# Optimization experiments

Hardware: AMD Instinct MI355X
Metric: run time of the kernel (lower is better)

## Reference

```python
import jax, jax.numpy as jnp
import numpy as np

B, N, D = 8, 2048, 256
K = 8
NP = 1024  # num_pooled = ceil(N * 0.5)
EPS = 1e-8
TEMP = 1.0


def setup_inputs() -> dict:
    key = jax.random.key(0)
    k1, k2, k3, k4 = jax.random.split(key, 4)
    tokens = jax.random.normal(k1, (B, N, D), dtype=jnp.float32)
    timestamps = jax.random.uniform(k2, (B, N), dtype=jnp.float32)
    W1 = jax.random.normal(k3, (2 * D, 128), dtype=jnp.float32) * 0.02
    b1 = jnp.zeros((128,), dtype=jnp.float32)
    W2 = jax.random.normal(k4, (128, NP), dtype=jnp.float32) * 0.02
    b2 = jnp.zeros((NP,), dtype=jnp.float32)
    return {"tokens": tokens, "timestamps": timestamps, "W1": W1, "b1": b1, "W2": W2, "b2": b2}


def _build_adjacency(tokens):
    # mutual-kNN graph on cosine similarity -> [B, N, N] float 0/1
    tn = tokens / (jnp.linalg.norm(tokens, axis=-1, keepdims=True) + EPS)
    sim = jnp.einsum("bnd,bmd->bnm", tn, tn)
    sim = jnp.where(jnp.eye(N, dtype=bool)[None], -jnp.inf, sim)  # no self (add_self=False)
    _, idx = jax.lax.top_k(sim, K)  # [B, N, K]
    bi = jnp.arange(B)[:, None, None]
    ri = jnp.arange(N)[None, :, None]
    adj = jnp.zeros((B, N, N), dtype=bool).at[bi, ri, idx].set(True)
    adj = adj & jnp.swapaxes(adj, 1, 2)  # mutual
    return adj.astype(jnp.float32)


def reference(tokens, timestamps, W1, b1, W2, b2):
    adjacency = _build_adjacency(tokens)

    # degree-normalized aggregation (use_gnn=True)
    degree = jnp.clip(adjacency.sum(axis=-1, keepdims=True), 1.0, None)
    agg = jnp.matmul(adjacency / degree, tokens)  # [B, N, D]
    features = jnp.concatenate([tokens, agg], axis=-1)  # [B, N, 2D]

    # assignment MLP (Linear -> exact GELU -> Linear), softmax over clusters
    h = jax.nn.gelu(features @ W1 + b1, approximate=False)
    logits = h @ W2 + b2  # [B, N, NP]
    assign = jax.nn.softmax(logits / TEMP, axis=-1)

    # soft-assignment pooling
    pooled_tokens = jnp.einsum("bnp,bnd->bpd", assign, tokens)  # [B, NP, D]
    pooled_t = jnp.einsum("bnp,bn->bp", assign, timestamps)  # [B, NP]

    # reorder pooled tokens by pooled timestamp
    sort_idx = jnp.argsort(pooled_t, axis=-1)
    pooled_tokens = jnp.take_along_axis(pooled_tokens, sort_idx[..., None], axis=1)
    pooled_t = jnp.take_along_axis(pooled_t, sort_idx, axis=1)

    # auxiliary losses
    assign_st = jnp.einsum("bnp,bmp->bnm", assign, assign)
    link_loss = jnp.mean((assign_st - adjacency) ** 2)
    entropy = jnp.mean(-jnp.sum(assign * jnp.log(assign + EPS), axis=-1))

    return pooled_tokens, pooled_t, link_loss, entropy
```

## Files before the change

### kernel.cpp

```cpp
#include <hip/hip_runtime.h>
#include <math.h>

#define B_ 8
#define N_ 2048
#define D_ 256
#define K_ 8
#define NP_ 1024
#define H_ 128
#define EPS_ 1e-8f
#define NEG_INF_ (-1e30f)

typedef unsigned int uint;
typedef unsigned short ushort;
typedef __attribute__((ext_vector_type(4))) float f32x4;
typedef __attribute__((ext_vector_type(8))) short short8;

__device__ __forceinline__ float gelu_exact(float x) {
    return 0.5f * x * (1.0f + erff(x * 0.70710678118654752440f));
}

__device__ __forceinline__ float dot4(float4 a, float4 b) {
    return a.x * b.x + a.y * b.y + a.z * b.z + a.w * b.w;
}

__device__ __forceinline__ ushort f2bf(float f) {
    uint u = __float_as_uint(f);
    u = (u + 0x7FFFu + ((u >> 16) & 1u)) >> 16;
    return (ushort)u;
}

__device__ __forceinline__ void gll16(const void* g, void* l) {
    __builtin_amdgcn_global_load_lds(
        (const __attribute__((address_space(1))) unsigned int*)g,
        (__attribute__((address_space(3))) unsigned int*)l, 16, 0, 0);
}

__device__ __forceinline__ float bsum256(float* red, int t, float v) {
    red[t] = v;
    __syncthreads();
#pragma unroll
    for (int s = 128; s > 0; s >>= 1) {
        if (t < s) red[t] += red[t + s];
        __syncthreads();
    }
    float r = red[0];
    __syncthreads();
    return r;
}

__device__ __forceinline__ float bmax256(float* red, int t, float v) {
    red[t] = v;
    __syncthreads();
#pragma unroll
    for (int s = 128; s > 0; s >>= 1) {
        if (t < s) red[t] = fmaxf(red[t], red[t + s]);
        __syncthreads();
    }
    float r = red[0];
    __syncthreads();
    return r;
}

__device__ __forceinline__ uint mono16(uint v) {
    return (v & 0x8000u) ? ((~v) & 0xFFFFu) : (v | 0x8000u);
}

__global__ __launch_bounds__(256) void k_norm(const float* __restrict__ tokens,
                                              float* __restrict__ tn,
                                              ushort* __restrict__ tnbf) {
    int row = blockIdx.x;
    int t = threadIdx.x;
    __shared__ float red[256];
    float x = tokens[(size_t)row * D_ + t];
    float ss = bsum256(red, t, x * x);
    float nrm = sqrtf(ss) + EPS_;
    float y = x / nrm;
    tn[(size_t)row * D_ + t] = y;
    tnbf[(size_t)row * D_ + t] = f2bf(y);
}

#define SCW_ 72
#define INSK_(L) { bool in_ = key > L; uint tm_ = L; L = in_ ? key : L; key = in_ ? tm_ : key; }
#define INS16_ INSK_(l0) INSK_(l1) INSK_(l2) INSK_(l3) INSK_(l4) INSK_(l5) INSK_(l6) INSK_(l7) \
               INSK_(l8) INSK_(l9) INSK_(l10) INSK_(l11) INSK_(l12) INSK_(l13) INSK_(l14) INSK_(l15)
#define INSM_ INSK_(m0) INSK_(m1) INSK_(m2) INSK_(m3) INSK_(m4) INSK_(m5) INSK_(m6) INSK_(m7) \
              INSK_(m8) INSK_(m9) INSK_(m10) INSK_(m11) INSK_(m12) INSK_(m13) INSK_(m14) INSK_(m15)

__global__ __launch_bounds__(256) void k_simtop(const ushort* __restrict__ tnbf,
                                                int* __restrict__ cands) {
    __shared__ __align__(16) char lds[43264];
    char* Bs = lds + 8192;
    ushort* sc = (ushort*)(lds + 40960);
    uint* mg = (uint*)(lds + 8192);

    int bid = blockIdx.x;
    int b = bid & 7;
    int panel = bid >> 3;
    int i0 = panel * 16;
    int t = threadIdx.x;
    int lane = t & 63;
    int wv = t >> 6;
    const char* tbb = (const char*)(tnbf + (size_t)b * N_ * D_);

#pragma unroll
    for (int c = 0; c < 2; ++c) {
        int e = (wv * 2 + c) * 64 + lane;
        int row = e >> 5, g = e & 31;
        gll16(tbb + (size_t)(i0 + row) * 512 + ((g ^ (row & 15)) << 4),
              lds + (wv * 2 + c) * 1024);
    }
#pragma unroll
    for (int c = 0; c < 8; ++c) {
        int e = (wv * 8 + c) * 64 + lane;
        int row = e >> 5, g = e & 31;
        gll16(tbb + (size_t)row * 512 + ((g ^ (row & 15)) << 4),
              Bs + (wv * 8 + c) * 1024);
    }
    asm volatile("s_waitcnt vmcnt(0)" ::: "memory");
    __syncthreads();

    int selrow = t >> 4;
    int selcs = t & 15;
    int gi = i0 + selrow;
    uint l0=0,l1=0,l2=0,l3=0,l4=0,l5=0,l6=0,l7=0,l8=0,l9=0,l10=0,l11=0,l12=0,l13=0,l14=0,l15=0;

    int arow = lane & 15;
    int brow = wv * 16 + (lane & 15);
    int scw = ((lane >> 4) * 4) * SCW_ + wv * 16 + (lane & 15);

    for (int jt = 0; jt < 32; ++jt) {
        f32x4 acc = (f32x4){0.f, 0.f, 0.f, 0.f};
#pragma unroll
        for (int ks = 0; ks < 8; ++ks) {
            int u = ks * 4 + (lane >> 4);
            short8 af = *(const short8*)(lds + arow * 512 + ((u ^ arow) << 4));
            short8 bf = *(const short8*)(Bs + brow * 512 + ((u ^ (lane & 15)) << 4));
            acc = __builtin_amdgcn_mfma_f32_16x16x32_bf16(af, bf, acc, 0, 0, 0);
        }
#pragma unroll
        for (int v = 0; v < 4; ++v) sc[scw + v * SCW_] = f2bf(acc[v]);
        __syncthreads();

        if (jt < 31) {
#pragma unroll
            for (int c = 0; c < 8; ++c) {
                int e = (wv * 8 + c) * 64 + lane;
                int row = e >> 5, g = e & 31;
                gll16(tbb + (size_t)((jt + 1) * 64 + row) * 512 + ((g ^ (row & 15)) << 4),
                      Bs + (wv * 8 + c) * 1024);
            }
        }
        int j0 = jt * 64;
        int sbase = selrow * SCW_;
#pragma unroll
        for (int jj = 0; jj < 4; ++jj) {
            int col = selcs + jj * 16;
            int j = j0 + col;
            uint sv = sc[sbase + col];
            if (j != gi) {
                uint key = (mono16(sv) << 16) | (65535u - (uint)j);
                if (key > l15) { INS16_ }
            }
        }
        asm volatile("s_waitcnt vmcnt(0)" ::: "memory");
        __syncthreads();
    }

    uint* ml = mg + (size_t)t * 17;
    ml[0]=l0; ml[1]=l1; ml[2]=l2; ml[3]=l3; ml[4]=l4; ml[5]=l5; ml[6]=l6; ml[7]=l7;
    ml[8]=l8; ml[9]=l9; ml[10]=l10; ml[11]=l11; ml[12]=l12; ml[13]=l13; ml[14]=l14; ml[15]=l15;
    __syncthreads();
    if (selcs == 0) {
        uint m0=0,m1=0,m2=0,m3=0,m4=0,m5=0,m6=0,m7=0,m8=0,m9=0,m10=0,m11=0,m12=0,m13=0,m14=0,m15=0;
        const uint* base = mg + (size_t)(selrow * 16) * 17;
#pragma unroll
        for (int s2 = 0; s2 < 16; ++s2) {
            const uint* lp = base + s2 * 17;
            for (int q = 0; q < 16; ++q) {
                uint key = lp[q];
                if (key <= m15) break;
                INSM_
            }
        }
        int* crow = cands + ((size_t)b * N_ + gi) * 16;
        crow[0]=(int)(65535u-(m0&0xFFFFu));   crow[1]=(int)(65535u-(m1&0xFFFFu));
        crow[2]=(int)(65535u-(m2&0xFFFFu));   crow[3]=(int)(65535u-(m3&0xFFFFu));
        crow[4]=(int)(65535u-(m4&0xFFFFu));   crow[5]=(int)(65535u-(m5&0xFFFFu));
        crow[6]=(int)(65535u-(m6&0xFFFFu));   crow[7]=(int)(65535u-(m7&0xFFFFu));
        crow[8]=(int)(65535u-(m8&0xFFFFu));   crow[9]=(int)(65535u-(m9&0xFFFFu));
        crow[10]=(int)(65535u-(m10&0xFFFFu)); crow[11]=(int)(65535u-(m11&0xFFFFu));
        crow[12]=(int)(65535u-(m12&0xFFFFu)); crow[13]=(int)(65535u-(m13&0xFFFFu));
        crow[14]=(int)(65535u-(m14&0xFFFFu)); crow[15]=(int)(65535u-(m15&0xFFFFu));
    }
}

__global__ __launch_bounds__(64) void k_rescore(const float* __restrict__ tn,
                                                const int* __restrict__ cands,
                                                int* __restrict__ topk) {
    int row = blockIdx.x;
    int b = row >> 11;
    int lane = threadIdx.x;
    int j = cands[(size_t)row * 16 + (lane & 15)];
    float s = 0.f;
    if (lane < 16) {
        const float* ti = tn + (size_t)row * D_;
        const float* tj = tn + ((size_t)(b << 11) + j) * D_;
        for (int d = 0; d < D_; d += 4) {
            float4 u = *(const float4*)(tj + d);
            float4 w = *(const float4*)(ti + d);
            s += dot4(u, w);
        }
    }
    float dv[16];
    int jv[16];
#pragma unroll
    for (int c = 0; c < 16; ++c) {
        dv[c] = __shfl(s, c);
        jv[c] = __shfl(j, c);
    }
    uint used = 0;
    for (int r = 0; r < 8; ++r) {
        float bv = -1e38f;
        int bj = 1 << 30, bc = -1;
#pragma unroll
        for (int c = 0; c < 16; ++c) {
            bool av = !(used & (1u << c));
            bool better = av && (dv[c] > bv || (dv[c] == bv && jv[c] < bj));
            bv = better ? dv[c] : bv;
            bj = better ? jv[c] : bj;
            bc = better ? c : bc;
        }
        used |= 1u << bc;
        if (lane == 0) topk[(size_t)row * K_ + r] = bj;
    }
}

__global__ __launch_bounds__(64) void k_adj_agg(const float* __restrict__ tokens,
                                                const int* __restrict__ topk,
                                                int* __restrict__ nbr,
                                                int* __restrict__ deg,
                                                float* __restrict__ agg) {
    int row = blockIdx.x;
    int b = row >> 11;
    int i = row & (N_ - 1);
    int t = threadIdx.x;
    __shared__ int s_cand[K_];
    __shared__ int s_nbr[K_];
    __shared__ int s_deg;
    if (t < K_) {
        int j = topk[(size_t)row * K_ + t];
        const int* tj = topk + ((size_t)(b * N_ + j)) * K_;
        bool mut = false;
#pragma unroll
        for (int k = 0; k < K_; ++k) mut = mut || (tj[k] == i);
        s_cand[t] = mut ? j : -1;
    }
    __syncthreads();
    if (t == 0) {
        int d = 0;
#pragma unroll
        for (int k = 0; k < K_; ++k)
            if (s_cand[k] >= 0) s_nbr[d++] = s_cand[k];
        s_deg = d;
    }
    __syncthreads();
    int dgi = s_deg;
    const float* tb = tokens + (size_t)b * N_ * D_;
    float a0 = 0, a1 = 0, a2 = 0, a3 = 0;
    for (int k = 0; k < dgi; ++k) {
        float4 v = *(const float4*)(tb + (size_t)s_nbr[k] * D_ + t * 4);
        a0 += v.x; a1 += v.y; a2 += v.z; a3 += v.w;
    }
    float inv = 1.0f / (float)(dgi > 0 ? dgi : 1);
    *(float4*)(agg + (size_t)row * D_ + t * 4) = make_float4(a0 * inv, a1 * inv, a2 * inv, a3 * inv);
    if (t < K_) nbr[(size_t)row * K_ + t] = (t < dgi) ? s_nbr[t] : -1;
    if (t == 0) deg[row] = dgi;
}

__global__ __launch_bounds__(256) void k_tokT(const float* __restrict__ tokens,
                                              ushort* __restrict__ tokT) {
    int b = blockIdx.z;
    int n0 = blockIdx.x * 32, d0 = blockIdx.y * 32;
    __shared__ float tile[32][33];
    int t = threadIdx.x;
#pragma unroll
    for (int q = 0; q < 4; ++q) {
        int e = q * 256 + t;
        int r = e >> 5, c = e & 31;
        tile[r][c] = tokens[((size_t)b * N_ + n0 + r) * D_ + d0 + c];
    }
    __syncthreads();
#pragma unroll
    for (int q = 0; q < 4; ++q) {
        int e = q * 256 + t;
        int r = e >> 5, c = e & 31;
        tokT[((size_t)b * D_ + d0 + r) * N_ + n0 + c] = f2bf(tile[c][r]);
    }
}

__global__ __launch_bounds__(256) void k_asT(const float* __restrict__ assign,
                                             ushort* __restrict__ assignT) {
    int b = blockIdx.z;
    int n0 = blockIdx.x * 32, p0 = blockIdx.y * 32;
    __shared__ float tile[32][33];
    int t = threadIdx.x;
#pragma unroll
    for (int q = 0; q < 4; ++q) {
        int e = q * 256 + t;
        int r = e >> 5, c = e & 31;
        tile[r][c] = assign[((size_t)b * N_ + n0 + r) * NP_ + p0 + c];
    }
    __syncthreads();
#pragma unroll
    for (int q = 0; q < 4; ++q) {
        int e = q * 256 + t;
        int r = e >> 5, c = e & 31;
        assignT[((size_t)b * NP_ + p0 + r) * N_ + n0 + c] = f2bf(tile[c][r]);
    }
}

__global__ __launch_bounds__(256) void k_mlp1(const float* __restrict__ tokens,
                                              const float* __restrict__ agg,
                                              const float* __restrict__ W1,
                                              const float* __restrict__ b1,
                                              float* __restrict__ h) {
    int row0 = blockIdx.x * 16;
    int t = threadIdx.x;
    int col = t & 127;
    int half = t >> 7;
    __shared__ float feat[16][2 * D_];
    for (int e = t; e < 16 * 2 * D_; e += 256) {
        int r = e >> 9, c = e & 511;
        feat[r][c] = (c < D_) ? tokens[(size_t)(row0 + r) * D_ + c]
                              : agg[(size_t)(row0 + r) * D_ + (c - D_)];
    }
    __syncthreads();
    const float* fr = &feat[half * 8][0];
    float bias = b1[col];
    float a0 = bias, a1 = bias, a2 = bias, a3 = bias, a4 = bias, a5 = bias, a6 = bias, a7 = bias;
    for (int i = 0; i < 2 * D_; i += 4) {
        float w0 = W1[(size_t)(i + 0) * H_ + col];
        float w1 = W1[(size_t)(i + 1) * H_ + col];
        float w2 = W1[(size_t)(i + 2) * H_ + col];
        float w3 = W1[(size_t)(i + 3) * H_ + col];
        float4 f0 = *(const float4*)(fr + 0 * 512 + i);
        float4 f1 = *(const float4*)(fr + 1 * 512 + i);
        float4 f2 = *(const float4*)(fr + 2 * 512 + i);
        float4 f3 = *(const float4*)(fr + 3 * 512 + i);
        float4 f4 = *(const float4*)(fr + 4 * 512 + i);
        float4 f5 = *(const float4*)(fr + 5 * 512 + i);
        float4 f6 = *(const float4*)(fr + 6 * 512 + i);
        float4 f7 = *(const float4*)(fr + 7 * 512 + i);
        a0 += f0.x * w0; a0 += f0.y * w1; a0 += f0.z * w2; a0 += f0.w * w3;
        a1 += f1.x * w0; a1 += f1.y * w1; a1 += f1.z * w2; a1 += f1.w * w3;
        a2 += f2.x * w0; a2 += f2.y * w1; a2 += f2.z * w2; a2 += f2.w * w3;
        a3 += f3.x * w0; a3 += f3.y * w1; a3 += f3.z * w2; a3 += f3.w * w3;
        a4 += f4.x * w0; a4 += f4.y * w1; a4 += f4.z * w2; a4 += f4.w * w3;
        a5 += f5.x * w0; a5 += f5.y * w1; a5 += f5.z * w2; a5 += f5.w * w3;
        a6 += f6.x * w0; a6 += f6.y * w1; a6 += f6.z * w2; a6 += f6.w * w3;
        a7 += f7.x * w0; a7 += f7.y * w1; a7 += f7.z * w2; a7 += f7.w * w3;
    }
    int rb = row0 + half * 8;
    h[(size_t)(rb + 0) * H_ + col] = gelu_exact(a0);
    h[(size_t)(rb + 1) * H_ + col] = gelu_exact(a1);
    h[(size_t)(rb + 2) * H_ + col] = gelu_exact(a2);
    h[(size_t)(rb + 3) * H_ + col] = gelu_exact(a3);
    h[(size_t)(rb + 4) * H_ + col] = gelu_exact(a4);
    h[(size_t)(rb + 5) * H_ + col] = gelu_exact(a5);
    h[(size_t)(rb + 6) * H_ + col] = gelu_exact(a6);
    h[(size_t)(rb + 7) * H_ + col] = gelu_exact(a7);
}

__global__ __launch_bounds__(256) void k_mlp2f(const float* __restrict__ hmat,
                                               const float* __restrict__ W2,
                                               const float* __restrict__ b2,
                                               float* __restrict__ assign,
                                               float* __restrict__ ent_partial) {
    int row0 = blockIdx.x * 16;
    int t = threadIdx.x;
    __shared__ float hsT[128 * 17];
    __shared__ float red2[16][256];
    __shared__ float red[256];
    for (int e = t; e < 16 * H_; e += 256) {
        int r = e >> 7, i = e & 127;
        hsT[i * 17 + r] = hmat[(size_t)row0 * H_ + e];
    }
    __syncthreads();
    float acc[16][4];
#pragma unroll
    for (int s = 0; s < 4; ++s) {
        float bb = b2[s * 256 + t];
#pragma unroll
        for (int r = 0; r < 16; ++r) acc[r][s] = bb;
    }
#pragma unroll 2
    for (int i = 0; i < H_; ++i) {
        float w0 = W2[(size_t)i * NP_ + t];
        float w1 = W2[(size_t)i * NP_ + 256 + t];
        float w2 = W2[(size_t)i * NP_ + 512 + t];
        float w3 = W2[(size_t)i * NP_ + 768 + t];
        float hv[16];
        *(float4*)&hv[0] = *(const float4*)&hsT[i * 17 + 0];
        *(float4*)&hv[4] = *(const float4*)&hsT[i * 17 + 4];
        *(float4*)&hv[8] = *(const float4*)&hsT[i * 17 + 8];
        *(float4*)&hv[12] = *(const float4*)&hsT[i * 17 + 12];
#pragma unroll
        for (int r = 0; r < 16; ++r) {
            acc[r][0] += hv[r] * w0; acc[r][1] += hv[r] * w1;
            acc[r][2] += hv[r] * w2; acc[r][3] += hv[r] * w3;
        }
    }
#pragma unroll
    for (int r = 0; r < 16; ++r)
        red2[r][t] = fmaxf(fmaxf(acc[r][0], acc[r][1]), fmaxf(acc[r][2], acc[r][3]));
    __syncthreads();
#pragma unroll
    for (int s = 128; s > 0; s >>= 1) {
        if (t < s) {
#pragma unroll
            for (int r = 0; r < 16; ++r) red2[r][t] = fmaxf(red2[r][t], red2[r][t + s]);
        }
        __syncthreads();
    }
#pragma unroll
    for (int r = 0; r < 16; ++r) {
        float m = red2[r][0];
        acc[r][0] -= m; acc[r][1] -= m; acc[r][2] -= m; acc[r][3] -= m;
    }
    __syncthreads();
#pragma unroll
    for (int r = 0; r < 16; ++r)
        red2[r][t] = expf(acc[r][0]) + expf(acc[r][1]) + expf(acc[r][2]) + expf(acc[r][3]);
    __syncthreads();
#pragma unroll
    for (int s = 128; s > 0; s >>= 1) {
        if (t < s) {
#pragma unroll
            for (int r = 0; r < 16; ++r) red2[r][t] += red2[r][t + s];
        }
        __syncthreads();
    }
    float entv = 0.f;
#pragma unroll
    for (int r = 0; r < 16; ++r) {
        float tot = red2[r][0];
        float inv = 1.0f / tot;
        float p0 = expf(acc[r][0]) * inv, p1 = expf(acc[r][1]) * inv;
        float p2 = expf(acc[r][2]) * inv, p3 = expf(acc[r][3]) * inv;
        float* arow = assign + (size_t)(row0 + r) * NP_;
        arow[t] = p0; arow[256 + t] = p1; arow[512 + t] = p2; arow[768 + t] = p3;
        entv -= p0 * logf(p0 + EPS_) + p1 * logf(p1 + EPS_) + p2 * logf(p2 + EPS_) + p3 * logf(p3 + EPS_);
    }
    float bs = bsum256(red, t, entv);
    if (t == 0) ent_partial[blockIdx.x] = bs;
}

__device__ __forceinline__ void stage8k(const ushort* __restrict__ A,
                                        const ushort* __restrict__ B,
                                        int kb, char* lA, char* lB, int wv, int lane) {
#pragma unroll
    for (int c = 0; c < 2; ++c) {
        int e = (wv * 2 + c) * 64 + lane;
        int row = e >> 3, g = e & 7;
        size_t go = (size_t)row * N_ + kb + ((g ^ (row & 7)) << 3);
        gll16(A + go, lA + (wv * 2 + c) * 1024);
        gll16(B + go, lB + (wv * 2 + c) * 1024);
    }
}

__device__ __forceinline__ void gemm64g(const ushort* __restrict__ A,
                                        const ushort* __restrict__ B,
                                        f32x4 acc[2][2], char* lds) {
    int t = threadIdx.x;
    int lane = t & 63;
    int wv = t >> 6;
    int wm = wv >> 1, wn = wv & 1;
    stage8k(A, B, 0, lds, lds + 8192, wv, lane);
    for (int kb = 0; kb < N_; kb += 64) {
        int cur = (kb >> 6) & 1;
        char* lA = lds + cur * 16384;
        char* lB = lA + 8192;
        asm volatile("s_waitcnt vmcnt(0)" ::: "memory");
        __syncthreads();
        if (kb + 64 < N_) {
            char* nA = lds + (cur ^ 1) * 16384;
            stage8k(A, B, kb + 64, nA, nA + 8192, wv, lane);
        }
#pragma unroll
        for (int ks = 0; ks < 2; ++ks) {
            short8 afr[2], bfr[2];
#pragma unroll
            for (int f = 0; f < 2; ++f) {
                int rowA = wm * 32 + f * 16 + (lane & 15);
                int u = ks * 4 + (lane >> 4);
                afr[f] = *(const short8*)(lA + rowA * 128 + ((u ^ (rowA & 7)) << 4));
                int rowB = wn * 32 + f * 16 + (lane & 15);
                bfr[f] = *(const short8*)(lB + rowB * 128 + ((u ^ (rowB & 7)) << 4));
            }
#pragma unroll
            for (int fm = 0; fm < 2; ++fm)
#pragma unroll
                for (int fn = 0; fn < 2; ++fn)
                    acc[fm][fn] = __builtin_amdgcn_mfma_f32_16x16x32_bf16(
                        afr[fm], bfr[fn], acc[fm][fn], 0, 0, 0);
        }
    }
}

__global__ __launch_bounds__(256) void k_pool64(const ushort* __restrict__ assignT,
                                                const ushort* __restrict__ tokT,
                                                float* __restrict__ pooled) {
    __shared__ __align__(16) char lds[32768];
    int bid = blockIdx.x;
    int b = bid & 7;
    int tile = bid >> 3;
    int p0 = (tile >> 2) * 64, d0 = (tile & 3) * 64;
    const ushort* A = assignT + ((size_t)b * NP_ + p0) * N_;
    const ushort* Bp = tokT + ((size_t)b * D_ + d0) * N_;
    f32x4 acc[2][2];
#pragma unroll
    for (int x = 0; x < 2; ++x)
#pragma unroll
        for (int y = 0; y < 2; ++y) acc[x][y] = (f32x4){0.f, 0.f, 0.f, 0.f};
    gemm64g(A, Bp, acc, lds);
    int lane = threadIdx.x & 63;
    int wid = threadIdx.x >> 6;
    int wm = wid >> 1, wn = wid & 1;
#pragma unroll
    for (int fm = 0; fm < 2; ++fm)
#pragma unroll
        for (int fn = 0; fn < 2; ++fn) {
            int p = p0 + wm * 32 + fm * 16 + (lane >> 4) * 4;
            int d = d0 + wn * 32 + fn * 16 + (lane & 15);
#pragma unroll
            for (int v = 0; v < 4; ++v)
                pooled[((size_t)b * NP_ + p + v) * D_ + d] = acc[fm][fn][v];
        }
}

__global__ __launch_bounds__(256) void k_gram64(const ushort* __restrict__ assignT,
                                                float* __restrict__ gram_partial) {
    __shared__ __align__(16) char lds[32768];
    __shared__ float red[256];
    int bid = blockIdx.x;
    int b = bid & 7;
    int idx = bid >> 3;
    int ti = 0, rem = idx;
    while (rem >= 16 - ti) { rem -= 16 - ti; ++ti; }
    int tj = ti + rem;
    const ushort* A = assignT + ((size_t)b * NP_ + ti * 64) * N_;
    const ushort* Bp = assignT + ((size_t)b * NP_ + tj * 64) * N_;
    f32x4 acc[2][2];
#pragma unroll
    for (int x = 0; x < 2; ++x)
#pragma unroll
        for (int y = 0; y < 2; ++y) acc[x][y] = (f32x4){0.f, 0.f, 0.f, 0.f};
    gemm64g(A, Bp, acc, lds);
    float lsum = 0.f;
#pragma unroll
    for (int x = 0; x < 2; ++x)
#pragma unroll
        for (int y = 0; y < 2; ++y)
#pragma unroll
            for (int v = 0; v < 4; ++v) lsum += acc[x][y][v] * acc[x][y][v];
    float bs = bsum256(red, threadIdx.x, lsum);
    if (threadIdx.x == 0) gram_partial[(size_t)b * 136 + idx] = (ti == tj ? 1.0f : 2.0f) * bs;
}

__global__ __launch_bounds__(256) void k_poolt_part(const float* __restrict__ assign,
                                                    const float* __restrict__ ts,
                                                    float* __restrict__ part) {
    int bid = blockIdx.x;
    int b = bid & 7, ck = bid >> 3;
    int t = threadIdx.x;
    const float* A = assign + ((size_t)b * N_ + (size_t)ck * 64) * NP_;
    const float* T = ts + (size_t)b * N_ + (size_t)ck * 64;
    float4 acc = make_float4(0.f, 0.f, 0.f, 0.f);
    for (int n = 0; n < 64; ++n) {
        float4 v = *(const float4*)(A + (size_t)n * NP_ + t * 4);
        float tv = T[n];
        acc.x += v.x * tv; acc.y += v.y * tv; acc.z += v.z * tv; acc.w += v.w * tv;
    }
    *(float4*)(part + ((size_t)(b * 32 + ck)) * NP_ + t * 4) = acc;
}

__global__ __launch_bounds__(256) void k_poolt_red(const float* __restrict__ part,
                                                   float* __restrict__ pooled_t_u) {
    int b = blockIdx.x;
    int t = threadIdx.x;
    float4 acc = make_float4(0.f, 0.f, 0.f, 0.f);
    for (int ck = 0; ck < 32; ++ck) {
        float4 v = *(const float4*)(part + ((size_t)(b * 32 + ck)) * NP_ + t * 4);
        acc.x += v.x; acc.y += v.y; acc.z += v.z; acc.w += v.w;
    }
    *(float4*)(pooled_t_u + (size_t)b * NP_ + t * 4) = acc;
}

__global__ __launch_bounds__(64) void k_edge(const float* __restrict__ assign,
                                             const int* __restrict__ nbr,
                                             const int* __restrict__ deg,
                                             float* __restrict__ edge_partial) {
    int row = blockIdx.x;
    int t = threadIdx.x;
    int dgi = deg[row];
    int b = row >> 11;
    float acc = 0.f;
    if (dgi > 0) {
        const float* ai = assign + (size_t)row * NP_;
        float areg[16];
#pragma unroll
        for (int q = 0; q < 16; ++q) areg[q] = ai[q * 64 + t];
        for (int k = 0; k < dgi; ++k) {
            int j = nbr[(size_t)row * K_ + k];
            const float* aj = assign + ((size_t)(b * N_ + j)) * NP_;
#pragma unroll
            for (int q = 0; q < 16; ++q) acc += areg[q] * aj[q * 64 + t];
        }
    }
#pragma unroll
    for (int s = 32; s > 0; s >>= 1) acc += __shfl_down(acc, s);
    if (t == 0) edge_partial[row] = acc;
}

__global__ __launch_bounds__(256) void k_sort(const float* __restrict__ pooled_t_u,
                                              float* __restrict__ out_pt,
                                              int* __restrict__ sortidx) {
    int b = blockIdx.x;
    int t = threadIdx.x;
    __shared__ float val[NP_];
    __shared__ int sidx[NP_];
    for (int e = t; e < NP_; e += 256) { val[e] = pooled_t_u[(size_t)b * NP_ + e]; sidx[e] = e; }
    __syncthreads();
    for (int k = 2; k <= NP_; k <<= 1) {
        for (int j = k >> 1; j > 0; j >>= 1) {
            for (int e = t; e < NP_; e += 256) {
                int l = e ^ j;
                if (l > e) {
                    bool up = ((e & k) == 0);
                    float v1 = val[e], v2 = val[l];
                    int i1 = sidx[e], i2 = sidx[l];
                    bool sw = up ? ((v1 > v2) || (v1 == v2 && i1 > i2))
                                 : ((v1 < v2) || (v1 == v2 && i1 < i2));
                    if (sw) { val[e] = v2; val[l] = v1; sidx[e] = i2; sidx[l] = i1; }
                }
            }
            __syncthreads();
        }
    }
    for (int e = t; e < NP_; e += 256) {
        out_pt[(size_t)b * NP_ + e] = val[e];
        sortidx[(size_t)b * NP_ + e] = sidx[e];
    }
}

__global__ __launch_bounds__(64) void k_gather(const float* __restrict__ pooledU,
                                               const int* __restrict__ sortidx,
                                               float* __restrict__ out) {
    int bp = blockIdx.x;
    int b = bp >> 10;
    int src = sortidx[bp];
    const float4* s = (const float4*)(pooledU + ((size_t)(b << 10) + src) * D_);
    float4* d = (float4*)(out + (size_t)bp * D_);
    d[threadIdx.x] = s[threadIdx.x];
}

__global__ __launch_bounds__(256) void k_fin(const float* __restrict__ gram_partial,
                                             const float* __restrict__ edge_partial,
                                             const float* __restrict__ ent_partial,
                                             const int* __restrict__ deg,
                                             float* __restrict__ out2) {
    int t = threadIdx.x;
    __shared__ float red[256];
    float t1 = 0.f, t2 = 0.f, t3 = 0.f, ent = 0.f;
    for (int i = t; i < 136 * B_; i += 256) t1 += gram_partial[i];
    for (int i = t; i < B_ * N_; i += 256) t2 += edge_partial[i];
    for (int i = t; i < (B_ * N_) / 16; i += 256) ent += ent_partial[i];
    for (int i = t; i < B_ * N_; i += 256) t3 += (float)deg[i];
    t1 = bsum256(red, t, t1);
    t2 = bsum256(red, t, t2);
    t3 = bsum256(red, t, t3);
    ent = bsum256(red, t, ent);
    if (t == 0) {
        out2[0] = (t1 - 2.f * t2 + t3) / (float)((size_t)B_ * N_ * N_);
        out2[1] = ent / (float)(B_ * N_);
    }
}

extern "C" void kernel_launch(void* const* d_in, const int* in_sizes, int n_in,
                              void* d_out, int out_size, void* d_ws, size_t ws_size,
                              hipStream_t stream) {
    const float* tokens = (const float*)d_in[0];
    const float* tstamp = (const float*)d_in[1];
    const float* W1 = (const float*)d_in[2];
    const float* b1 = (const float*)d_in[3];
    const float* W2 = (const float*)d_in[4];
    const float* b2 = (const float*)d_in[5];
    float* out = (float*)d_out;

    char* wsp = (char*)d_ws;
    size_t off = 0;
    auto alloc = [&](size_t bytes) -> void* {
        void* p = wsp + off;
        off += (bytes + 255) & ~(size_t)255;
        return p;
    };
    float* tn = (float*)alloc(sizeof(float) * (size_t)B_ * N_ * D_);
    float* agg = tn;
    float* assign = (float*)alloc(sizeof(float) * (size_t)B_ * N_ * NP_);
    ushort* tnbf = (ushort*)alloc(sizeof(ushort) * (size_t)B_ * N_ * D_);
    ushort* tokT = tnbf;
    float* hbuf = (float*)alloc(sizeof(float) * (size_t)B_ * N_ * H_);
    ushort* assignT = (ushort*)alloc(sizeof(ushort) * (size_t)B_ * NP_ * N_);
    float* pooledU = (float*)alloc(sizeof(float) * (size_t)B_ * NP_ * D_);
    float* pooltU = (float*)alloc(sizeof(float) * (size_t)B_ * NP_);
    float* poolt_part = (float*)alloc(sizeof(float) * (size_t)B_ * 32 * NP_);
    int* candbuf = (int*)alloc(sizeof(int) * (size_t)B_ * N_ * 16);
    int* topkbuf = (int*)alloc(sizeof(int) * (size_t)B_ * N_ * K_);
    int* nbrbuf = (int*)alloc(sizeof(int) * (size_t)B_ * N_ * K_);
    int* degbuf = (int*)alloc(sizeof(int) * (size_t)B_ * N_);
    int* sortidx = (int*)alloc(sizeof(int) * (size_t)B_ * NP_);
    float* gram_p = (float*)alloc(sizeof(float) * 136 * B_);
    float* edge_p = (float*)alloc(sizeof(float) * (size_t)B_ * N_);
    float* ent_p = (float*)alloc(sizeof(float) * (size_t)(B_ * N_) / 16);

    k_norm<<<B_ * N_, 256, 0, stream>>>(tokens, tn, tnbf);
    k_simtop<<<1024, 256, 0, stream>>>(tnbf, candbuf);
    k_rescore<<<B_ * N_, 64, 0, stream>>>(tn, candbuf, topkbuf);
    k_adj_agg<<<B_ * N_, 64, 0, stream>>>(tokens, topkbuf, nbrbuf, degbuf, agg);
    k_tokT<<<dim3(N_ / 32, D_ / 32, B_), 256, 0, stream>>>(tokens, tokT);
    k_mlp1<<<(B_ * N_) / 16, 256, 0, stream>>>(tokens, agg, W1, b1, hbuf);
    k_mlp2f<<<(B_ * N_) / 16, 256, 0, stream>>>(hbuf, W2, b2, assign, ent_p);
    k_asT<<<dim3(N_ / 32, NP_ / 32, B_), 256, 0, stream>>>(assign, assignT);
    k_pool64<<<512, 256, 0, stream>>>(assignT, tokT, pooledU);
    k_poolt_part<<<256, 256, 0, stream>>>(assign, tstamp, poolt_part);
    k_poolt_red<<<B_, 256, 0, stream>>>(poolt_part, pooltU);
    k_gram64<<<1088, 256, 0, stream>>>(assignT, gram_p);
    k_edge<<<B_ * N_, 64, 0, stream>>>(assign, nbrbuf, degbuf, edge_p);
    k_sort<<<B_, 256, 0, stream>>>(pooltU, out + (size_t)B_ * NP_ * D_, sortidx);
    k_gather<<<B_ * NP_, 64, 0, stream>>>(pooledU, sortidx, out);
    k_fin<<<1, 256, 0, stream>>>(gram_p, edge_p, ent_p, degbuf,
                                 out + (size_t)B_ * NP_ * D_ + (size_t)B_ * NP_);
}
```

Measured before the change: 604.5 us.

## Triple-buffer GEMM staging, share top-k thresholds, pad MLP2 LDS, precompute load pointers

The shared gemm64g used by pooling and the Gram kernel moves from double to triple buffering with partial vmcnt waits, so two tiles can be in flight while MFMA runs. This costs more LDS per block (48KB) and an extra barrier per iteration. In k_simtop, a per-row shared threshold updated by atomicMax lets the 16 lanes of a row skip insertion work sooner, and global-load pointers are computed once and then incremented. k_mlp2f pads the transposed h tile to a stride of 20 so float4 LDS reads stay aligned, and unrolls its loop further.

```diff
diff --git a/kernel.cpp b/kernel.cpp
--- a/kernel.cpp
+++ b/kernel.cpp
@@ -89,6 +89,7 @@
 __global__ __launch_bounds__(256) void k_simtop(const ushort* __restrict__ tnbf,
                                                 int* __restrict__ cands) {
     __shared__ __align__(16) char lds[43264];
+    __shared__ uint rowTh[16];
     char* Bs = lds + 8192;
     ushort* sc = (ushort*)(lds + 40960);
     uint* mg = (uint*)(lds + 8192);
@@ -101,6 +102,8 @@
     int lane = t & 63;
     int wv = t >> 6;
     const char* tbb = (const char*)(tnbf + (size_t)b * N_ * D_);
+
+    if (t < 16) rowTh[t] = 0;
 
 #pragma unroll
     for (int c = 0; c < 2; ++c) {
@@ -109,12 +112,17 @@
         gll16(tbb + (size_t)(i0 + row) * 512 + ((g ^ (row & 15)) << 4),
               lds + (wv * 2 + c) * 1024);
     }
+    const char* gsrc[8];
 #pragma unroll
     for (int c = 0; c < 8; ++c) {
         int e = (wv * 8 + c) * 64 + lane;
         int row = e >> 5, g = e & 31;
-        gll16(tbb + (size_t)row * 512 + ((g ^ (row & 15)) << 4),
-              Bs + (wv * 8 + c) * 1024);
+        gsrc[c] = tbb + (size_t)row * 512 + ((g ^ (row & 15)) << 4);
+    }
+#pragma unroll
+    for (int c = 0; c < 8; ++c) {
+        gll16(gsrc[c], Bs + (wv * 8 + c) * 1024);
+        gsrc[c] += 32768;
     }
     asm volatile("s_waitcnt vmcnt(0)" ::: "memory");
     __syncthreads();
@@ -144,14 +152,14 @@
         if (jt < 31) {
 #pragma unroll
             for (int c = 0; c < 8; ++c) {
-                int e = (wv * 8 + c) * 64 + lane;
-                int row = e >> 5, g = e & 31;
-                gll16(tbb + (size_t)((jt + 1) * 64 + row) * 512 + ((g ^ (row & 15)) << 4),
-                      Bs + (wv * 8 + c) * 1024);
+                gll16(gsrc[c], Bs + (wv * 8 + c) * 1024);
+                gsrc[c] += 32768;
             }
         }
         int j0 = jt * 64;
         int sbase = selrow * SCW_;
+        uint rth = rowTh[selrow];
+        uint gate = l15 > rth ? l15 : rth;
 #pragma unroll
         for (int jj = 0; jj < 4; ++jj) {
             int col = selcs + jj * 16;
@@ -159,9 +167,13 @@
             uint sv = sc[sbase + col];
             if (j != gi) {
                 uint key = (mono16(sv) << 16) | (65535u - (uint)j);
-                if (key > l15) { INS16_ }
+                if (key > gate) {
+                    INS16_
+                    gate = l15 > rth ? l15 : rth;
+                }
             }
         }
+        atomicMax(&rowTh[selrow], l15);
         asm volatile("s_waitcnt vmcnt(0)" ::: "memory");
         __syncthreads();
     }
@@ -378,12 +390,12 @@
                                                float* __restrict__ ent_partial) {
     int row0 = blockIdx.x * 16;
     int t = threadIdx.x;
-    __shared__ float hsT[128 * 17];
+    __shared__ float hsT[128 * 20];
     __shared__ float red2[16][256];
     __shared__ float red[256];
     for (int e = t; e < 16 * H_; e += 256) {
         int r = e >> 7, i = e & 127;
-        hsT[i * 17 + r] = hmat[(size_t)row0 * H_ + e];
+        hsT[i * 20 + r] = hmat[(size_t)row0 * H_ + e];
     }
     __syncthreads();
     float acc[16][4];
@@ -393,17 +405,17 @@
 #pragma unroll
         for (int r = 0; r < 16; ++r) acc[r][s] = bb;
     }
-#pragma unroll 2
+#pragma unroll 4
     for (int i = 0; i < H_; ++i) {
         float w0 = W2[(size_t)i * NP_ + t];
         float w1 = W2[(size_t)i * NP_ + 256 + t];
         float w2 = W2[(size_t)i * NP_ + 512 + t];
         float w3 = W2[(size_t)i * NP_ + 768 + t];
         float hv[16];
-        *(float4*)&hv[0] = *(const float4*)&hsT[i * 17 + 0];
-        *(float4*)&hv[4] = *(const float4*)&hsT[i * 17 + 4];
-        *(float4*)&hv[8] = *(const float4*)&hsT[i * 17 + 8];
-        *(float4*)&hv[12] = *(const float4*)&hsT[i * 17 + 12];
+        *(float4*)&hv[0] = *(const float4*)&hsT[i * 20 + 0];
+        *(float4*)&hv[4] = *(const float4*)&hsT[i * 20 + 4];
+        *(float4*)&hv[8] = *(const float4*)&hsT[i * 20 + 8];
+        *(float4*)&hv[12] = *(const float4*)&hsT[i * 20 + 12];
 #pragma unroll
         for (int r = 0; r < 16; ++r) {
             acc[r][0] += hv[r] * w0; acc[r][1] += hv[r] * w1;
@@ -455,37 +467,56 @@
     if (t == 0) ent_partial[blockIdx.x] = bs;
 }
 
-__device__ __forceinline__ void stage8k(const ushort* __restrict__ A,
+__device__ __forceinline__ void gemm64g(const ushort* __restrict__ A,
                                         const ushort* __restrict__ B,
-                                        int kb, char* lA, char* lB, int wv, int lane) {
+                                        f32x4 acc[2][2], char* lds) {
+    int t = threadIdx.x;
+    int lane = t & 63;
+    int wv = t >> 6;
+    int wm = wv >> 1, wn = wv & 1;
+    const char* pA[2];
+    const char* pB[2];
+    int ldo[2];
 #pragma unroll
     for (int c = 0; c < 2; ++c) {
         int e = (wv * 2 + c) * 64 + lane;
         int row = e >> 3, g = e & 7;
-        size_t go = (size_t)row * N_ + kb + ((g ^ (row & 7)) << 3);
-        gll16(A + go, lA + (wv * 2 + c) * 1024);
-        gll16(B + go, lB + (wv * 2 + c) * 1024);
-    }
-}
-
-__device__ __forceinline__ void gemm64g(const ushort* __restrict__ A,
-                                        const ushort* __restrict__ B,
-                                        f32x4 acc[2][2], char* lds) {
-    int t = threadIdx.x;
-    int lane = t & 63;
-    int wv = t >> 6;
-    int wm = wv >> 1, wn = wv & 1;
-    stage8k(A, B, 0, lds, lds + 8192, wv, lane);
-    for (int kb = 0; kb < N_; kb += 64) {
-        int cur = (kb >> 6) & 1;
+        size_t go = (size_t)row * (N_ * 2) + ((g ^ (row & 7)) << 4);
+        pA[c] = (const char*)A + go;
+        pB[c] = (const char*)B + go;
+        ldo[c] = (wv * 2 + c) * 1024;
+    }
+#pragma unroll
+    for (int q = 0; q < 2; ++q) {
+#pragma unroll
+        for (int c = 0; c < 2; ++c) {
+            gll16(pA[c], lds + q * 16384 + ldo[c]);
+            gll16(pB[c], lds + q * 16384 + 8192 + ldo[c]);
+            pA[c] += 128;
+            pB[c] += 128;
+        }
+    }
+    int cur = 0;
+    for (int kb = 0; kb < 32; ++kb) {
         char* lA = lds + cur * 16384;
         char* lB = lA + 8192;
-        asm volatile("s_waitcnt vmcnt(0)" ::: "memory");
+        if (kb < 30) {
+            int nq = cur + 2; if (nq >= 3) nq -= 3;
+            char* nb = lds + nq * 16384;
+#pragma unroll
+            for (int c = 0; c < 2; ++c) {
+                gll16(pA[c], nb + ldo[c]);
+                gll16(pB[c], nb + 8192 + ldo[c]);
+                pA[c] += 128;
+                pB[c] += 128;
+            }
+            asm volatile("s_waitcnt vmcnt(8)" ::: "memory");
+        } else if (kb == 30) {
+            asm volatile("s_waitcnt vmcnt(4)" ::: "memory");
+        } else {
+            asm volatile("s_waitcnt vmcnt(0)" ::: "memory");
+        }
         __syncthreads();
-        if (kb + 64 < N_) {
-            char* nA = lds + (cur ^ 1) * 16384;
-            stage8k(A, B, kb + 64, nA, nA + 8192, wv, lane);
-        }
 #pragma unroll
         for (int ks = 0; ks < 2; ++ks) {
             short8 afr[2], bfr[2];
@@ -504,13 +535,15 @@
                     acc[fm][fn] = __builtin_amdgcn_mfma_f32_16x16x32_bf16(
                         afr[fm], bfr[fn], acc[fm][fn], 0, 0, 0);
         }
+        __syncthreads();
+        ++cur; if (cur == 3) cur = 0;
     }
 }
 
 __global__ __launch_bounds__(256) void k_pool64(const ushort* __restrict__ assignT,
                                                 const ushort* __restrict__ tokT,
                                                 float* __restrict__ pooled) {
-    __shared__ __align__(16) char lds[32768];
+    __shared__ __align__(16) char lds[49152];
     int bid = blockIdx.x;
     int b = bid & 7;
     int tile = bid >> 3;
@@ -540,7 +573,7 @@
 
 __global__ __launch_bounds__(256) void k_gram64(const ushort* __restrict__ assignT,
                                                 float* __restrict__ gram_partial) {
-    __shared__ __align__(16) char lds[32768];
+    __shared__ __align__(16) char lds[49152];
     __shared__ float red[256];
     int bid = blockIdx.x;
     int b = bid & 7;
```

New measurement: 630.0 us. +4.2%, slower.
